# Kernel optimization log

Hardware: AMD Instinct MI355X
Metric: run time of the kernel (lower is better)

Reference implementation:

```python
import jax, jax.numpy as jnp
import numpy as np

B, S, D = 2, 2048, 1024
H = 16
HD = D // H  # 64
SCALE = HD ** -0.5


def setup_inputs() -> dict:
    key = jax.random.key(0)
    ks = jax.random.split(key, 9)
    init = lambda k, shape: jax.random.normal(k, shape, dtype=jnp.float32) * (1.0 / np.sqrt(shape[-1]))
    return {
        "x": jax.random.normal(ks[0], (B, S, D), dtype=jnp.float32),
        "wq": init(ks[1], (D, D)), "bq": jnp.zeros((D,), jnp.float32),
        "wk": init(ks[2], (D, D)), "bk": jnp.zeros((D,), jnp.float32),
        "wv": init(ks[3], (D, D)), "bv": jnp.zeros((D,), jnp.float32),
        "wo": init(ks[4], (D, D)), "bo": jnp.zeros((D,), jnp.float32),
    }


def reference(x, wq, bq, wk, bk, wv, bv, wo, bo):
    b, s, d = x.shape
    # projections -> [b, h, s, hd]
    q = (x @ wq + bq).reshape(b, s, H, HD).transpose(0, 2, 1, 3)
    k = (x @ wk + bk).reshape(b, s, H, HD).transpose(0, 2, 1, 3)
    v = (x @ wv + bv).reshape(b, s, H, HD).transpose(0, 2, 1, 3)
    # full causal attention (chunked loop in original computes exactly this)
    scores = jnp.einsum("bhqd,bhkd->bhqk", q, k) * SCALE
    causal = jnp.tril(jnp.ones((s, s), dtype=bool))
    scores = jnp.where(causal, scores, -jnp.inf)
    weights = jax.nn.softmax(scores, axis=-1)
    out = jnp.einsum("bhqk,bhkd->bhqd", weights, v)
    out = out.transpose(0, 2, 1, 3).reshape(b, s, d)
    return out @ wo + bo
```

## Files before the change

kernel.cpp:

```cpp
#include <hip/hip_runtime.h>
#include <hip/hip_bf16.h>
#include <cstdint>

#define B_  2
#define S_  2048
#define D_  1024
#define H_  16
#define HD_ 64
#define M_  (B_ * S_)
static constexpr float SC_LOG2E = 0.125f * 1.44269504088896f;

typedef __bf16 bf16x8 __attribute__((ext_vector_type(8)));
typedef __bf16 bf16x4 __attribute__((ext_vector_type(4)));
typedef float  f32x4  __attribute__((ext_vector_type(4)));

__device__ __forceinline__ unsigned short f2b(float f) {
  union { float f; unsigned u; } x; x.f = f;
  unsigned r = x.u + 0x7FFF + ((x.u >> 16) & 1);
  return (unsigned short)(r >> 16);
}

__device__ __forceinline__ void gl_lds16(const unsigned short* g, unsigned short* l) {
  __builtin_amdgcn_global_load_lds((const __attribute__((address_space(1))) void*)g,
                                   (__attribute__((address_space(3))) void*)l, 16, 0, 0);
}

__global__ void cvt_all_kernel(const float* __restrict__ x,
                               const float* __restrict__ w0, const float* __restrict__ w1,
                               const float* __restrict__ w2, const float* __restrict__ w3,
                               unsigned short* __restrict__ xb,
                               unsigned short* __restrict__ o0, unsigned short* __restrict__ o1,
                               unsigned short* __restrict__ o2, unsigned short* __restrict__ o3) {
  int tx = threadIdx.x, ty = threadIdx.y;
  if (blockIdx.z == 4) {
    int tid = ty * 32 + tx;
    int base = ((int)blockIdx.y * 32 + (int)blockIdx.x) * 1024 + tid;
    const float4* xf = (const float4*)x;
    ushort4* ob = (ushort4*)xb;
#pragma unroll
    for (int j = 0; j < 4; j++) {
      float4 v = xf[base + j * 256];
      ushort4 r;
      r.x = f2b(v.x); r.y = f2b(v.y); r.z = f2b(v.z); r.w = f2b(v.w);
      ob[base + j * 256] = r;
    }
    return;
  }
  const float* w = blockIdx.z == 0 ? w0 : blockIdx.z == 1 ? w1 : blockIdx.z == 2 ? w2 : w3;
  unsigned short* o = blockIdx.z == 0 ? o0 : blockIdx.z == 1 ? o1 : blockIdx.z == 2 ? o2 : o3;
  __shared__ float t[32][33];
  int x0 = blockIdx.x * 32, y0 = blockIdx.y * 32;
#pragma unroll
  for (int j = 0; j < 4; j++)
    t[ty + j * 8][tx] = w[(size_t)(y0 + ty + j * 8) * D_ + x0 + tx];
  __syncthreads();
#pragma unroll
  for (int j = 0; j < 4; j++)
    o[(size_t)(x0 + ty + j * 8) * D_ + y0 + tx] = f2b(t[tx][ty + j * 8]);
}

__global__ __launch_bounds__(512) void qkv_gemm_kernel(
    const unsigned short* __restrict__ xb,
    const unsigned short* __restrict__ wqt, const unsigned short* __restrict__ wkt,
    const unsigned short* __restrict__ wvt,
    const float* __restrict__ bq, const float* __restrict__ bk, const float* __restrict__ bv,
    unsigned short* __restrict__ qo, unsigned short* __restrict__ ko, unsigned short* __restrict__ vo) {
  const unsigned short* wt = blockIdx.z == 0 ? wqt : blockIdx.z == 1 ? wkt : wvt;
  const float* bias        = blockIdx.z == 0 ? bq  : blockIdx.z == 1 ? bk  : bv;
  unsigned short* out      = blockIdx.z == 0 ? qo  : blockIdx.z == 1 ? ko  : vo;
  const float scl = blockIdx.z == 0 ? SC_LOG2E : 1.0f;

  __shared__ __align__(16) unsigned short smem[4 * 128 * 32];
  const int tid = threadIdx.x;
  const int lane = tid & 63, wid = tid >> 6;
  const int wm = wid & 1, wn = wid >> 1;
  const int m0 = blockIdx.x * 128, n0 = blockIdx.y * 128;
  const int l15 = lane & 15, q4 = lane >> 4;
  const int srow = tid >> 2, skc = (tid & 3) * 8;

  f32x4 zero = {0.f, 0.f, 0.f, 0.f};
  f32x4 acc[4][2];
#pragma unroll
  for (int mt = 0; mt < 4; mt++)
#pragma unroll
    for (int nt = 0; nt < 2; nt++) acc[mt][nt] = zero;

  gl_lds16(xb + (size_t)(m0 + srow) * D_ + skc, smem + tid * 8);
  gl_lds16(wt + (size_t)(n0 + srow) * D_ + skc, smem + 8192 + tid * 8);

  int ib = 0;
  for (int kk = 0; kk < D_; kk += 32, ib ^= 1) {
    unsigned short* Ab = smem + ib * 4096;
    unsigned short* Bb = smem + 8192 + ib * 4096;
    unsigned short* An = smem + (ib ^ 1) * 4096;
    unsigned short* Bn = smem + 8192 + (ib ^ 1) * 4096;
    __syncthreads();
    if (kk + 32 < D_) {
      gl_lds16(xb + (size_t)(m0 + srow) * D_ + kk + 32 + skc, An + tid * 8);
      gl_lds16(wt + (size_t)(n0 + srow) * D_ + kk + 32 + skc, Bn + tid * 8);
    }
    bf16x8 af[4], bfv[2];
#pragma unroll
    for (int mt = 0; mt < 4; mt++) af[mt]  = *(const bf16x8*)(Ab + (wm * 64 + mt * 16 + l15) * 32 + q4 * 8);
#pragma unroll
    for (int nt = 0; nt < 2; nt++) bfv[nt] = *(const bf16x8*)(Bb + (wn * 32 + nt * 16 + l15) * 32 + q4 * 8);
#pragma unroll
    for (int mt = 0; mt < 4; mt++)
#pragma unroll
      for (int nt = 0; nt < 2; nt++)
        acc[mt][nt] = __builtin_amdgcn_mfma_f32_16x16x32_bf16(af[mt], bfv[nt], acc[mt][nt], 0, 0, 0);
  }

  if (blockIdx.z < 2) {
#pragma unroll
    for (int nt = 0; nt < 2; nt++) {
      int n = n0 + wn * 32 + nt * 16 + l15;
      float bn = bias[n];
      int h = n >> 6, hd = n & 63;
#pragma unroll
      for (int mt = 0; mt < 4; mt++) {
#pragma unroll
        for (int r = 0; r < 4; r++) {
          int m = m0 + wm * 64 + mt * 16 + q4 * 4 + r;
          int b = m >> 11, s = m & (S_ - 1);
          out[(((size_t)(b * H_ + h)) * S_ + s) * HD_ + hd] = f2b((acc[mt][nt][r] + bn) * scl);
        }
      }
    }
  } else {
    unsigned short* buf = smem;
#pragma unroll
    for (int p = 0; p < 2; p++) {
      __syncthreads();
      if ((wn >> 1) == p) {
#pragma unroll
        for (int nt = 0; nt < 2; nt++) {
          int np = (wn & 1) * 32 + nt * 16 + l15;
          float bn = bias[n0 + p * 64 + np];
#pragma unroll
          for (int mt = 0; mt < 4; mt++) {
            f32x4 vb = acc[mt][nt];
            vb[0] += bn; vb[1] += bn; vb[2] += bn; vb[3] += bn;
            bf16x4 pk = __builtin_convertvector(vb, bf16x4);
            *(bf16x4*)(&buf[np * 136 + wm * 64 + mt * 16 + q4 * 4]) = pk;
          }
        }
      }
      __syncthreads();
#pragma unroll
      for (int i = 0; i < 2; i++) {
        int ci = tid + i * 512;
        int np = ci >> 4, c = ci & 15;
        int n = n0 + p * 64 + np;
        int h = n >> 6, hd = n & 63;
        int m = m0 + c * 8;
        int b = m >> 11, s = m & (S_ - 1);
        *(uint4*)(out + (((size_t)(b * H_ + h)) * HD_ + hd) * S_ + s) = *(const uint4*)(buf + np * 136 + c * 8);
      }
    }
  }
}

__global__ __launch_bounds__(512) void attn_kernel(
    const unsigned short* __restrict__ Q, const unsigned short* __restrict__ K,
    const unsigned short* __restrict__ Vt_g, unsigned short* __restrict__ O) {
  const int bh = blockIdx.y, b = bh >> 4, h = bh & 15;
  const unsigned short* Qh = Q    + (size_t)bh * S_ * HD_;
  const unsigned short* Kh = K    + (size_t)bh * S_ * HD_;
  const unsigned short* Vh = Vt_g + (size_t)bh * HD_ * S_;

  __shared__ __align__(16) unsigned short Ks[2][128 * 72];
  __shared__ __align__(16) unsigned short Vt[2][64 * 136];
  __shared__ __align__(16) unsigned short Ps[8][16 * 136];

  const int tid = threadIdx.x, lane = tid & 63, w = tid >> 6;
  const int l15 = lane & 15, q4 = lane >> 4;
  f32x4 zero = {0.f, 0.f, 0.f, 0.f};

  const int krow0 = tid >> 3, kcol0 = (tid & 7) * 8;
  const int vrow0 = tid >> 4, vcol0 = (tid & 15) * 8;

  int tc = 0;
  for (int half = 0; half < 2; half++) {
    const int qi = half ? (15 - (int)blockIdx.x) : (int)blockIdx.x;
    const int q0 = qi * 128;

    const unsigned short* qp = Qh + (size_t)(q0 + w * 16 + l15) * HD_ + q4 * 8;
    bf16x8 bq0 = *(const bf16x8*)(qp);
    bf16x8 bq1 = *(const bf16x8*)(qp + 32);

    float m_i = -1e30f, l_i = 0.f;
    f32x4 o_acc[4];
#pragma unroll
    for (int t = 0; t < 4; t++) o_acc[t] = zero;
    const int qrow = q0 + w * 16 + l15;
    const int nkt = qi + 1;

    uint4 kp0 = *(const uint4*)(Kh + (size_t)krow0 * HD_ + kcol0);
    uint4 kp1 = *(const uint4*)(Kh + (size_t)(krow0 + 64) * HD_ + kcol0);
    uint4 vp0 = *(const uint4*)(Vh + (size_t)vrow0 * S_ + vcol0);
    uint4 vp1 = *(const uint4*)(Vh + (size_t)(vrow0 + 32) * S_ + vcol0);

    for (int kt = 0; kt < nkt; kt++, tc++) {
      const int k0 = kt * 128;
      const int bi = tc & 1;
      unsigned short* Kb = Ks[bi];
      unsigned short* Vb = Vt[bi];
      *(uint4*)(Kb + krow0 * 72 + kcol0) = kp0;
      *(uint4*)(Kb + (krow0 + 64) * 72 + kcol0) = kp1;
      *(uint4*)(Vb + vrow0 * 136 + vcol0) = vp0;
      *(uint4*)(Vb + (vrow0 + 32) * 136 + vcol0) = vp1;
      __syncthreads();
      if (kt + 1 < nkt) {
        int kn = k0 + 128;
        kp0 = *(const uint4*)(Kh + (size_t)(kn + krow0) * HD_ + kcol0);
        kp1 = *(const uint4*)(Kh + (size_t)(kn + krow0 + 64) * HD_ + kcol0);
        vp0 = *(const uint4*)(Vh + (size_t)vrow0 * S_ + kn + vcol0);
        vp1 = *(const uint4*)(Vh + (size_t)(vrow0 + 32) * S_ + kn + vcol0);
      }

      f32x4 sc[8];
#pragma unroll
      for (int nt = 0; nt < 8; nt++) sc[nt] = zero;
#pragma unroll
      for (int nt = 0; nt < 8; nt++) {
        bf16x8 ak0 = *(const bf16x8*)(Kb + (nt * 16 + l15) * 72 + q4 * 8);
        bf16x8 ak1 = *(const bf16x8*)(Kb + (nt * 16 + l15) * 72 + 32 + q4 * 8);
        sc[nt] = __builtin_amdgcn_mfma_f32_16x16x32_bf16(ak0, bq0, sc[nt], 0, 0, 0);
        sc[nt] = __builtin_amdgcn_mfma_f32_16x16x32_bf16(ak1, bq1, sc[nt], 0, 0, 0);
      }

      const bool needMask = (k0 + 127) > (q0 + w * 16);
      float mx = m_i;
      if (needMask) {
#pragma unroll
        for (int nt = 0; nt < 8; nt++)
#pragma unroll
          for (int r = 0; r < 4; r++) {
            int key = k0 + nt * 16 + q4 * 4 + r;
            float v = (key > qrow) ? -1e30f : sc[nt][r];
            sc[nt][r] = v;
            mx = fmaxf(mx, v);
          }
      } else {
#pragma unroll
        for (int nt = 0; nt < 8; nt++)
#pragma unroll
          for (int r = 0; r < 4; r++) mx = fmaxf(mx, sc[nt][r]);
      }
      mx = fmaxf(mx, __shfl_xor(mx, 16));
      mx = fmaxf(mx, __shfl_xor(mx, 32));
      float alpha = __builtin_amdgcn_exp2f(m_i - mx);
      m_i = mx;
      float rs = 0.f;
#pragma unroll
      for (int nt = 0; nt < 8; nt++)
#pragma unroll
        for (int r = 0; r < 4; r++) {
          float p = __builtin_amdgcn_exp2f(sc[nt][r] - mx);
          sc[nt][r] = p;
          rs += p;
        }
      rs += __shfl_xor(rs, 16);
      rs += __shfl_xor(rs, 32);
      l_i = l_i * alpha + rs;

#pragma unroll
      for (int r = 0; r < 4; r++) {
        float ar = __shfl(alpha, q4 * 4 + r);
        o_acc[0][r] *= ar; o_acc[1][r] *= ar; o_acc[2][r] *= ar; o_acc[3][r] *= ar;
      }

#pragma unroll
      for (int nt = 0; nt < 8; nt++) {
        bf16x4 pk = __builtin_convertvector(sc[nt], bf16x4);
        *(bf16x4*)(&Ps[w][l15 * 136 + nt * 16 + q4 * 4]) = pk;
      }
      __threadfence_block();

#pragma unroll
      for (int ks = 0; ks < 4; ks++) {
        bf16x8 ap = *(const bf16x8*)(&Ps[w][l15 * 136 + ks * 32 + q4 * 8]);
#pragma unroll
        for (int nt2 = 0; nt2 < 4; nt2++) {
          bf16x8 bv = *(const bf16x8*)(Vb + (nt2 * 16 + l15) * 136 + ks * 32 + q4 * 8);
          o_acc[nt2] = __builtin_amdgcn_mfma_f32_16x16x32_bf16(ap, bv, o_acc[nt2], 0, 0, 0);
        }
      }
    }

#pragma unroll
    for (int r = 0; r < 4; r++) {
      float lr = __shfl(l_i, q4 * 4 + r);
      float inv = 1.0f / lr;
      int s = q0 + w * 16 + q4 * 4 + r;
#pragma unroll
      for (int nt2 = 0; nt2 < 4; nt2++)
        O[((size_t)(b * S_ + s)) * D_ + h * HD_ + nt2 * 16 + l15] = f2b(o_acc[nt2][r] * inv);
    }
  }
}

__global__ __launch_bounds__(512) void out_gemm_kernel(
    const unsigned short* __restrict__ ab, const unsigned short* __restrict__ wot,
    const float* __restrict__ bo, float* __restrict__ out) {
  __shared__ __align__(16) unsigned short smem[4 * 128 * 32];
  const int tid = threadIdx.x;
  const int lane = tid & 63, wid = tid >> 6;
  const int wm = wid & 1, wn = wid >> 1;
  const int m0 = blockIdx.x * 128, n0 = blockIdx.y * 128;
  const int l15 = lane & 15, q4 = lane >> 4;
  const int srow = tid >> 2, skc = (tid & 3) * 8;

  f32x4 zero = {0.f, 0.f, 0.f, 0.f};
  f32x4 acc[4][2];
#pragma unroll
  for (int mt = 0; mt < 4; mt++)
#pragma unroll
    for (int nt = 0; nt < 2; nt++) acc[mt][nt] = zero;

  gl_lds16(ab  + (size_t)(m0 + srow) * D_ + skc, smem + tid * 8);
  gl_lds16(wot + (size_t)(n0 + srow) * D_ + skc, smem + 8192 + tid * 8);

  int ib = 0;
  for (int kk = 0; kk < D_; kk += 32, ib ^= 1) {
    unsigned short* Ab = smem + ib * 4096;
    unsigned short* Bb = smem + 8192 + ib * 4096;
    unsigned short* An = smem + (ib ^ 1) * 4096;
    unsigned short* Bn = smem + 8192 + (ib ^ 1) * 4096;
    __syncthreads();
    if (kk + 32 < D_) {
      gl_lds16(ab  + (size_t)(m0 + srow) * D_ + kk + 32 + skc, An + tid * 8);
      gl_lds16(wot + (size_t)(n0 + srow) * D_ + kk + 32 + skc, Bn + tid * 8);
    }
    bf16x8 af[4], bfv[2];
#pragma unroll
    for (int mt = 0; mt < 4; mt++) af[mt]  = *(const bf16x8*)(Ab + (wm * 64 + mt * 16 + l15) * 32 + q4 * 8);
#pragma unroll
    for (int nt = 0; nt < 2; nt++) bfv[nt] = *(const bf16x8*)(Bb + (wn * 32 + nt * 16 + l15) * 32 + q4 * 8);
#pragma unroll
    for (int mt = 0; mt < 4; mt++)
#pragma unroll
      for (int nt = 0; nt < 2; nt++)
        acc[mt][nt] = __builtin_amdgcn_mfma_f32_16x16x32_bf16(af[mt], bfv[nt], acc[mt][nt], 0, 0, 0);
  }

#pragma unroll
  for (int nt = 0; nt < 2; nt++) {
    int n = n0 + wn * 32 + nt * 16 + l15;
    float bn = bo[n];
#pragma unroll
    for (int mt = 0; mt < 4; mt++) {
#pragma unroll
      for (int r = 0; r < 4; r++) {
        int m = m0 + wm * 64 + mt * 16 + q4 * 4 + r;
        out[(size_t)m * D_ + n] = acc[mt][nt][r] + bn;
      }
    }
  }
}

extern "C" void kernel_launch(void* const* d_in, const int* in_sizes, int n_in,
                              void* d_out, int out_size, void* d_ws, size_t ws_size,
                              hipStream_t stream) {
  const float* x  = (const float*)d_in[0];
  const float* wq = (const float*)d_in[1];
  const float* bq = (const float*)d_in[2];
  const float* wk = (const float*)d_in[3];
  const float* bk = (const float*)d_in[4];
  const float* wv = (const float*)d_in[5];
  const float* bv = (const float*)d_in[6];
  const float* wo = (const float*)d_in[7];
  const float* bo = (const float*)d_in[8];
  float* out = (float*)d_out;

  char* ws = (char*)d_ws;
  unsigned short* xb  = (unsigned short*)(ws);
  unsigned short* wqt = (unsigned short*)(ws + (8u  << 20));
  unsigned short* wkt = (unsigned short*)(ws + (10u << 20));
  unsigned short* wvt = (unsigned short*)(ws + (12u << 20));
  unsigned short* wot = (unsigned short*)(ws + (14u << 20));
  unsigned short* qb  = (unsigned short*)(ws + (16u << 20));
  unsigned short* kb  = (unsigned short*)(ws + (24u << 20));
  unsigned short* vtg = (unsigned short*)(ws + (32u << 20));
  unsigned short* ab  = xb;

  cvt_all_kernel<<<dim3(32, 32, 5), dim3(32, 8), 0, stream>>>(x, wq, wk, wv, wo, xb, wqt, wkt, wvt, wot);
  qkv_gemm_kernel<<<dim3(32, 8, 3), dim3(512), 0, stream>>>(xb, wqt, wkt, wvt, bq, bk, bv, qb, kb, vtg);
  attn_kernel<<<dim3(8, B_ * H_), dim3(512), 0, stream>>>(qb, kb, vtg, ab);
  out_gemm_kernel<<<dim3(32, 8), dim3(512), 0, stream>>>(ab, wot, bo, out);
}
```

Measured before the change: 180.3 us.

## Triple-buffer GEMM LDS loads with partial vmcnt waits and lighter attention barrier

Both projection GEMMs move from double to triple buffering in LDS, issuing global-to-LDS loads two k-steps ahead. Each step waits only until at most two loads are outstanding before the barrier, instead of a full __syncthreads drain, so one tile's memory latency can overlap compute on the previous tile. The attention kernel's barrier after the LDS stores becomes an lgkmcnt-only wait, so the register prefetch of the next K/V tile no longer has to finish first. The cost is more LDS per block (48KB), which may lower occupancy, and hand-written waitcnt barriers that depend on the exact count of outstanding loads.

```diff
diff --git a/kernel.cpp b/kernel.cpp
--- a/kernel.cpp
+++ b/kernel.cpp
@@ -23,6 +23,16 @@
 __device__ __forceinline__ void gl_lds16(const unsigned short* g, unsigned short* l) {
   __builtin_amdgcn_global_load_lds((const __attribute__((address_space(1))) void*)g,
                                    (__attribute__((address_space(3))) void*)l, 16, 0, 0);
+}
+
+__device__ __forceinline__ void bar_lgkm() {
+  asm volatile("s_waitcnt lgkmcnt(0)\n\ts_barrier" ::: "memory");
+}
+__device__ __forceinline__ void bar_vm2() {
+  asm volatile("s_waitcnt vmcnt(2) lgkmcnt(0)\n\ts_barrier" ::: "memory");
+}
+__device__ __forceinline__ void bar_vm0() {
+  asm volatile("s_waitcnt vmcnt(0) lgkmcnt(0)\n\ts_barrier" ::: "memory");
 }
 
 __global__ void cvt_all_kernel(const float* __restrict__ x,
@@ -70,7 +80,7 @@
   unsigned short* out      = blockIdx.z == 0 ? qo  : blockIdx.z == 1 ? ko  : vo;
   const float scl = blockIdx.z == 0 ? SC_LOG2E : 1.0f;
 
-  __shared__ __align__(16) unsigned short smem[4 * 128 * 32];
+  __shared__ __align__(16) unsigned short smem[6 * 4096];
   const int tid = threadIdx.x;
   const int lane = tid & 63, wid = tid >> 6;
   const int wm = wid & 1, wn = wid >> 1;
@@ -85,20 +95,23 @@
 #pragma unroll
     for (int nt = 0; nt < 2; nt++) acc[mt][nt] = zero;
 
-  gl_lds16(xb + (size_t)(m0 + srow) * D_ + skc, smem + tid * 8);
-  gl_lds16(wt + (size_t)(n0 + srow) * D_ + skc, smem + 8192 + tid * 8);
-
-  int ib = 0;
-  for (int kk = 0; kk < D_; kk += 32, ib ^= 1) {
-    unsigned short* Ab = smem + ib * 4096;
-    unsigned short* Bb = smem + 8192 + ib * 4096;
-    unsigned short* An = smem + (ib ^ 1) * 4096;
-    unsigned short* Bn = smem + 8192 + (ib ^ 1) * 4096;
-    __syncthreads();
-    if (kk + 32 < D_) {
-      gl_lds16(xb + (size_t)(m0 + srow) * D_ + kk + 32 + skc, An + tid * 8);
-      gl_lds16(wt + (size_t)(n0 + srow) * D_ + kk + 32 + skc, Bn + tid * 8);
-    }
+  const unsigned short* ap = xb + (size_t)(m0 + srow) * D_ + skc;
+  const unsigned short* bp = wt + (size_t)(n0 + srow) * D_ + skc;
+  gl_lds16(ap,      smem + tid * 8);
+  gl_lds16(bp,      smem + 12288 + tid * 8);
+  gl_lds16(ap + 32, smem + 4096 + tid * 8);
+  gl_lds16(bp + 32, smem + 12288 + 4096 + tid * 8);
+
+  int bc = 0;
+  for (int it = 0; it < 32; it++) {
+    if (it < 31) bar_vm2(); else bar_vm0();
+    if (it + 2 < 32) {
+      int bn_ = bc < 1 ? bc + 2 : bc - 1;
+      gl_lds16(ap + (it + 2) * 32, smem + bn_ * 4096 + tid * 8);
+      gl_lds16(bp + (it + 2) * 32, smem + 12288 + bn_ * 4096 + tid * 8);
+    }
+    const unsigned short* Ab = smem + bc * 4096;
+    const unsigned short* Bb = smem + 12288 + bc * 4096;
     bf16x8 af[4], bfv[2];
 #pragma unroll
     for (int mt = 0; mt < 4; mt++) af[mt]  = *(const bf16x8*)(Ab + (wm * 64 + mt * 16 + l15) * 32 + q4 * 8);
@@ -109,6 +122,7 @@
 #pragma unroll
       for (int nt = 0; nt < 2; nt++)
         acc[mt][nt] = __builtin_amdgcn_mfma_f32_16x16x32_bf16(af[mt], bfv[nt], acc[mt][nt], 0, 0, 0);
+    bc = bc == 2 ? 0 : bc + 1;
   }
 
   if (blockIdx.z < 2) {
@@ -210,7 +224,7 @@
       *(uint4*)(Kb + (krow0 + 64) * 72 + kcol0) = kp1;
       *(uint4*)(Vb + vrow0 * 136 + vcol0) = vp0;
       *(uint4*)(Vb + (vrow0 + 32) * 136 + vcol0) = vp1;
-      __syncthreads();
+      bar_lgkm();
       if (kt + 1 < nkt) {
         int kn = k0 + 128;
         kp0 = *(const uint4*)(Kh + (size_t)(kn + krow0) * HD_ + kcol0);
@@ -304,7 +318,7 @@
 __global__ __launch_bounds__(512) void out_gemm_kernel(
     const unsigned short* __restrict__ ab, const unsigned short* __restrict__ wot,
     const float* __restrict__ bo, float* __restrict__ out) {
-  __shared__ __align__(16) unsigned short smem[4 * 128 * 32];
+  __shared__ __align__(16) unsigned short smem[6 * 4096];
   const int tid = threadIdx.x;
   const int lane = tid & 63, wid = tid >> 6;
   const int wm = wid & 1, wn = wid >> 1;
@@ -319,20 +333,23 @@
 #pragma unroll
     for (int nt = 0; nt < 2; nt++) acc[mt][nt] = zero;
 
-  gl_lds16(ab  + (size_t)(m0 + srow) * D_ + skc, smem + tid * 8);
-  gl_lds16(wot + (size_t)(n0 + srow) * D_ + skc, smem + 8192 + tid * 8);
-
-  int ib = 0;
-  for (int kk = 0; kk < D_; kk += 32, ib ^= 1) {
-    unsigned short* Ab = smem + ib * 4096;
-    unsigned short* Bb = smem + 8192 + ib * 4096;
-    unsigned short* An = smem + (ib ^ 1) * 4096;
-    unsigned short* Bn = smem + 8192 + (ib ^ 1) * 4096;
-    __syncthreads();
-    if (kk + 32 < D_) {
-      gl_lds16(ab  + (size_t)(m0 + srow) * D_ + kk + 32 + skc, An + tid * 8);
-      gl_lds16(wot + (size_t)(n0 + srow) * D_ + kk + 32 + skc, Bn + tid * 8);
-    }
+  const unsigned short* ap = ab  + (size_t)(m0 + srow) * D_ + skc;
+  const unsigned short* bp = wot + (size_t)(n0 + srow) * D_ + skc;
+  gl_lds16(ap,      smem + tid * 8);
+  gl_lds16(bp,      smem + 12288 + tid * 8);
+  gl_lds16(ap + 32, smem + 4096 + tid * 8);
+  gl_lds16(bp + 32, smem + 12288 + 4096 + tid * 8);
+
+  int bc = 0;
+  for (int it = 0; it < 32; it++) {
+    if (it < 31) bar_vm2(); else bar_vm0();
+    if (it + 2 < 32) {
+      int bn_ = bc < 1 ? bc + 2 : bc - 1;
+      gl_lds16(ap + (it + 2) * 32, smem + bn_ * 4096 + tid * 8);
+      gl_lds16(bp + (it + 2) * 32, smem + 12288 + bn_ * 4096 + tid * 8);
+    }
+    const unsigned short* Ab = smem + bc * 4096;
+    const unsigned short* Bb = smem + 12288 + bc * 4096;
     bf16x8 af[4], bfv[2];
 #pragma unroll
     for (int mt = 0; mt < 4; mt++) af[mt]  = *(const bf16x8*)(Ab + (wm * 64 + mt * 16 + l15) * 32 + q4 * 8);
@@ -343,6 +360,7 @@
 #pragma unroll
       for (int nt = 0; nt < 2; nt++)
         acc[mt][nt] = __builtin_amdgcn_mfma_f32_16x16x32_bf16(af[mt], bfv[nt], acc[mt][nt], 0, 0, 0);
+    bc = bc == 2 ? 0 : bc + 1;
   }
 
 #pragma unroll
```

New measurement: 178.7 us. No clear change (-0.9%).
